# Kernel tuning notes

Hardware: AMD Instinct MI355X
Metric: run time of the kernel (lower is better)

Reference implementation:

```python
import jax, jax.numpy as jnp
import numpy as np
from jax import lax

SQRT_HALF = 0.7071067811865476
LAYERS = 20
STACKS = 2
LAYERS_PER_STACK = LAYERS // STACKS
K = 3
OUT_CH = 256
RES_CH = 64
GATE_CH = 128
SKIP_CH = 256
CIN_CH = 80


def setup_inputs() -> dict:
    key = jax.random.key(0)
    ks = jax.random.split(key, 20)
    s = 0.05
    inp = {
        'x': jax.random.normal(ks[0], (4, OUT_CH, 16384), jnp.float32),
        'c': jax.random.normal(ks[1], (4, CIN_CH, 16384), jnp.float32),
        # first conv: kernel size 2 (Conv1d2x1), out_channels -> residual_channels
        'W_first': jax.random.normal(ks[2], (RES_CH, OUT_CH, 2), jnp.float32) * s,
        'b_first': jnp.zeros((RES_CH,), jnp.float32),
        # per-layer dilated conv (residual -> gate), stacked over layers
        'W_dil': jax.random.normal(ks[3], (LAYERS, GATE_CH, RES_CH, K), jnp.float32) * s,
        'b_dil': jnp.zeros((LAYERS, GATE_CH), jnp.float32),
        # per-layer local-conditioning 1x1 (cin -> gate)
        'W_c': jax.random.normal(ks[4], (LAYERS, GATE_CH, CIN_CH), jnp.float32) * s,
        'b_c': jnp.zeros((LAYERS, GATE_CH), jnp.float32),
        # per-layer 1x1 skip (gate/2 -> skip) and out (gate/2 -> residual)
        'W_skip': jax.random.normal(ks[5], (LAYERS, SKIP_CH, GATE_CH // 2), jnp.float32) * s,
        'b_skip': jnp.zeros((LAYERS, SKIP_CH), jnp.float32),
        'W_out': jax.random.normal(ks[6], (LAYERS, RES_CH, GATE_CH // 2), jnp.float32) * s,
        'b_out': jnp.zeros((LAYERS, RES_CH), jnp.float32),
        # final 1x1 convs
        'W_last1': jax.random.normal(ks[7], (SKIP_CH, SKIP_CH), jnp.float32) * s,
        'b_last1': jnp.zeros((SKIP_CH,), jnp.float32),
        'W_last2': jax.random.normal(ks[8], (OUT_CH, SKIP_CH), jnp.float32) * s,
        'b_last2': jnp.zeros((OUT_CH,), jnp.float32),
    }
    return inp


def reference(x, c, W_first, b_first, W_dil, b_dil, W_c, b_c,
              W_skip, b_skip, W_out, b_out, W_last1, b_last1, W_last2, b_last2):
    dn = ('NCH', 'OIH', 'NCH')
    # first conv: F.pad(x, (1,0)) then kernel-2 conv == causal left pad 1
    h = lax.conv_general_dilated(x, W_first, (1,), [(1, 0)], dimension_numbers=dn)
    h = jnp.tanh(h + b_first[None, :, None])  # hparams.use_tanh_embed
    skips = None
    for l in range(LAYERS):
        d = 2 ** (l % LAYERS_PER_STACK)
        # causal dilated conv: pad left (K-1)*d
        y = lax.conv_general_dilated(h, W_dil[l], (1,), [((K - 1) * d, 0)],
                                     rhs_dilation=(d,), dimension_numbers=dn)
        y = y + b_dil[l][None, :, None]
        cond = jnp.einsum('bct,gc->bgt', c, W_c[l]) + b_c[l][None, :, None]
        a, b = jnp.split(y + cond, 2, axis=1)  # gated activation units
        z = jnp.tanh(a) * jax.nn.sigmoid(b)
        s = jnp.einsum('bgt,sg->bst', z, W_skip[l]) + b_skip[l][None, :, None]
        h = (jnp.einsum('bgt,rg->brt', z, W_out[l]) + b_out[l][None, :, None] + h) * SQRT_HALF
        if skips is None:
            skips = s
        else:
            skips = (skips + s) * SQRT_HALF  # faithful to original accumulation
    out = jax.nn.relu(skips)
    out = jnp.einsum('bst,os->bot', out, W_last1) + b_last1[None, :, None]
    out = jax.nn.relu(out)
    out = jnp.einsum('bst,os->bot', out, W_last2) + b_last2[None, :, None]
    return out
```

## Files before the change

### kernel.cpp

```cpp
#include <hip/hip_runtime.h>
#include <math.h>


#define T_LEN   16384
#define NB      4
#define BT      (NB * T_LEN)
#define NLAYERS 20
#define SQH     0.70710678118654752440f

typedef _Float16 half8 __attribute__((ext_vector_type(8)));
typedef _Float16 half4 __attribute__((ext_vector_type(4)));
typedef float f32x4 __attribute__((ext_vector_type(4)));

__device__ inline f32x4 mfma16(half8 a, half8 b, f32x4 c) {
  return __builtin_amdgcn_mfma_f32_16x16x32_f16(a, b, c, 0, 0, 0);
}

__global__ __launch_bounds__(256) void prep_pack(
    const float* __restrict__ Wf, const float* __restrict__ Wdil,
    const float* __restrict__ Wc, const float* __restrict__ Wskip,
    const float* __restrict__ Wout, const float* __restrict__ Wl1,
    const float* __restrict__ Wl2, const float* __restrict__ bdil,
    const float* __restrict__ bc, const float* __restrict__ bskip,
    _Float16* __restrict__ wdp, _Float16* __restrict__ wcp,
    _Float16* __restrict__ wop, _Float16* __restrict__ wskp,
    _Float16* __restrict__ wfp, _Float16* __restrict__ wl1p,
    _Float16* __restrict__ wl2p, float* __restrict__ bde,
    float* __restrict__ bsk)
{
  const float Q = 0.70710678118654752440f;
  const int WDP_E = 20 * 3 * 128 * 64;
  const int WCP_E = 20 * 128 * 96;
  const int WOP_E = 20 * 64 * 64;
  const int WSK_E = 256 * 1280;
  const int WFP_E = 64 * 512;
  const int WL_E  = 256 * 256;
  const int BDE_E = 20 * 128;
  const int BSK_E = 256;
  const int TOTAL = WDP_E + WCP_E + WOP_E + WSK_E + WFP_E + 2 * WL_E + BDE_E + BSK_E;
  for (int i = blockIdx.x * blockDim.x + threadIdx.x; i < TOTAL;
       i += gridDim.x * blockDim.x) {
    int j = i;
    if (j < WDP_E) {
      int l = j / (3 * 128 * 64); int r2 = j % (3 * 128 * 64);
      int tau = r2 / (128 * 64);  int r3 = r2 % (128 * 64);
      int n = r3 >> 6; int kc = r3 & 63;
      wdp[j] = (_Float16)Wdil[((l * 128 + n) * 64 + kc) * 3 + tau];
      continue;
    }
    j -= WDP_E;
    if (j < WCP_E) {
      int l = j / (128 * 96); int r2 = j % (128 * 96);
      int n = r2 / 96; int kc = r2 % 96;
      wcp[j] = (_Float16)(kc < 80 ? Wc[(l * 128 + n) * 80 + kc] : 0.f);
      continue;
    }
    j -= WCP_E;
    if (j < WOP_E) {
      int l = j >> 12; int r2 = j & 4095;
      int n = r2 >> 6; int kc = r2 & 63;
      wop[j] = (_Float16)Wout[(l * 64 + n) * 64 + kc];
      continue;
    }
    j -= WOP_E;
    if (j < WSK_E) {
      int n = j / 1280; int k = j % 1280;
      int l = k >> 6; int kc = k & 63;
      float f = (l == 0) ? 1.f : powf(Q, (float)(1 - l));
      wskp[j] = (_Float16)(Wskip[(l * 256 + n) * 64 + kc] * f);
      continue;
    }
    j -= WSK_E;
    if (j < WFP_E) {
      int n = j >> 9; int k = j & 511;
      int tau = k >> 8; int ci = k & 255;
      wfp[j] = (_Float16)Wf[(n * 256 + ci) * 2 + tau];
      continue;
    }
    j -= WFP_E;
    if (j < WL_E) { wl1p[j] = (_Float16)Wl1[j]; continue; }
    j -= WL_E;
    if (j < WL_E) { wl2p[j] = (_Float16)Wl2[j]; continue; }
    j -= WL_E;
    if (j < BDE_E) { bde[j] = bdil[j] + bc[j]; continue; }
    j -= BDE_E;
    {
      int n = j;
      float s = 0.f;
      for (int l = 0; l < NLAYERS; ++l) {
        float w = powf(Q, (float)(l == 0 ? 19 : 20 - l));
        s += bskip[l * 256 + n] * w;
      }
      bsk[n] = s;
    }
  }
}

__global__ __launch_bounds__(256) void tr_kernel(
    const float* __restrict__ src, _Float16* __restrict__ dst, int C, int Cpad, int CB)
{
  __shared__ float tile[32 * 33];
  int bid = blockIdx.x;
  int cb = bid % CB;
  int tb = (bid / CB) % (T_LEN / 32);
  int bb = bid / (CB * (T_LEN / 32));
  int t0 = tb * 32, ch0 = cb * 32;
  int tl = threadIdx.x & 31, cl = threadIdx.x >> 5;
#pragma unroll
  for (int i = 0; i < 4; ++i) {
    int ch = cl + 8 * i;
    float v = (ch0 + ch < C) ? src[((size_t)bb * C + ch0 + ch) * T_LEN + t0 + tl] : 0.f;
    tile[ch * 33 + tl] = v;
  }
  __syncthreads();
  int t = threadIdx.x >> 3;
  int c4 = (threadIdx.x & 7) * 4;
  half4 hv = {(_Float16)tile[(c4 + 0) * 33 + t], (_Float16)tile[(c4 + 1) * 33 + t],
              (_Float16)tile[(c4 + 2) * 33 + t], (_Float16)tile[(c4 + 3) * 33 + t]};
  *(half4*)&dst[((size_t)bb * T_LEN + t0 + t) * Cpad + ch0 + c4] = hv;
}

__global__ __launch_bounds__(256, 4) void first_conv(
    const _Float16* __restrict__ xt, const _Float16* __restrict__ wfp,
    const float* __restrict__ bf, _Float16* __restrict__ h0)
{
  __shared__ _Float16 As[128 * 72];
  __shared__ _Float16 Bs[64 * 72];
  const int tid = threadIdx.x;
  const int lane = tid & 63, w = tid >> 6;
  const int wx = w & 1, wy = w >> 1;
  const int l15 = lane & 15, quad = lane >> 4;
  const int p0 = blockIdx.x * 128;
  const int b = p0 >> 14, t0 = p0 & (T_LEN - 1);
  const int r = tid >> 1, halfo = (tid & 1) * 32;

  f32x4 acc[4][2];
#pragma unroll
  for (int mi = 0; mi < 4; ++mi)
#pragma unroll
    for (int ni = 0; ni < 2; ++ni) { f32x4 z = {0.f, 0.f, 0.f, 0.f}; acc[mi][ni] = z; }

  for (int s = 0; s < 8; ++s) {
    int tau = s >> 2, ci0 = (s & 3) * 64;
    int ts = t0 + r - 1 + tau;
    if (ts >= 0) {
      const uint4* src = (const uint4*)(xt + ((size_t)(b * T_LEN + ts) * 256 + ci0 + halfo));
#pragma unroll
      for (int j = 0; j < 4; ++j) *(uint4*)&As[r * 72 + halfo + 8 * j] = src[j];
    } else {
      uint4 z = {0, 0, 0, 0};
#pragma unroll
      for (int j = 0; j < 4; ++j) *(uint4*)&As[r * 72 + halfo + 8 * j] = z;
    }
    if (tid < 128) {
      const uint4* s4 = (const uint4*)(wfp + ((size_t)r * 512 + tau * 256 + ci0 + halfo));
#pragma unroll
      for (int j = 0; j < 4; ++j) *(uint4*)&Bs[r * 72 + halfo + 8 * j] = s4[j];
    }
    __syncthreads();
#pragma unroll
    for (int kc = 0; kc < 2; ++kc) {
      const int k0 = kc * 32 + quad * 8;
      half8 af[4], bfr[2];
#pragma unroll
      for (int mi = 0; mi < 4; ++mi)
        af[mi] = *(const half8*)&As[(64 * wy + 16 * mi + l15) * 72 + k0];
#pragma unroll
      for (int ni = 0; ni < 2; ++ni)
        bfr[ni] = *(const half8*)&Bs[(32 * wx + 16 * ni + l15) * 72 + k0];
#pragma unroll
      for (int mi = 0; mi < 4; ++mi)
#pragma unroll
        for (int ni = 0; ni < 2; ++ni)
          acc[mi][ni] = mfma16(af[mi], bfr[ni], acc[mi][ni]);
    }
    __syncthreads();
  }
#pragma unroll
  for (int mi = 0; mi < 4; ++mi)
#pragma unroll
    for (int ni = 0; ni < 2; ++ni) {
      int col = 32 * wx + 16 * ni + l15;
      int rowb = 64 * wy + 16 * mi + quad * 4;
      float bo = bf[col];
      size_t base = ((size_t)p0 + rowb) * 64 + col;
#pragma unroll
      for (int reg = 0; reg < 4; ++reg) {
        float v = acc[mi][ni][reg] + bo;
        float e = __expf(2.f * v);
        h0[base + (size_t)64 * reg] = (_Float16)(1.f - 2.f * __builtin_amdgcn_rcpf(e + 1.f));
      }
    }
}

__global__ __launch_bounds__(512, 4) void layer_kernel(
    const _Float16* __restrict__ hprev, _Float16* __restrict__ hnext,
    const _Float16* __restrict__ ctp,
    const _Float16* __restrict__ wdp_l, const _Float16* __restrict__ wcp_l,
    const _Float16* __restrict__ wop_l,
    const float* __restrict__ bde_l, const float* __restrict__ bout_l,
    _Float16* __restrict__ zslot, int d)
{
  __shared__ _Float16 As[128 * 72];
  __shared__ _Float16 Bs[128 * 72];
  __shared__ float bde_s[128];

  const int tid = threadIdx.x;
  const int lane = tid & 63, w = tid >> 6;
  const int wx = w & 1, wy = w >> 1;
  const int l15 = lane & 15, quad = lane >> 4;
  const int p0 = blockIdx.x * 128;
  const int b = p0 >> 14, t0 = p0 & (T_LEN - 1);
  const int r2 = tid >> 2, qo = (tid & 3) * 16;
  const int o8 = (tid & 3) * 8;

  if (tid < 128) bde_s[tid] = bde_l[tid];

  f32x4 acc[2][4];
#pragma unroll
  for (int mi = 0; mi < 2; ++mi)
#pragma unroll
    for (int ni = 0; ni < 4; ++ni) { f32x4 z = {0.f, 0.f, 0.f, 0.f}; acc[mi][ni] = z; }

  for (int s = 0; s < 5; ++s) {
    if (s < 3) {
      int ts = t0 + r2 - (2 - s) * d;
      if (ts >= 0) {
        const uint4* src = (const uint4*)(hprev + ((size_t)(b * T_LEN + ts) * 64 + qo));
        *(uint4*)&As[r2 * 72 + qo] = src[0];
        *(uint4*)&As[r2 * 72 + qo + 8] = src[1];
      } else {
        uint4 z4 = {0, 0, 0, 0};
        *(uint4*)&As[r2 * 72 + qo] = z4;
        *(uint4*)&As[r2 * 72 + qo + 8] = z4;
      }
      const uint4* sb = (const uint4*)(wdp_l + ((size_t)s * 8192 + r2 * 64 + qo));
      *(uint4*)&Bs[r2 * 72 + qo] = sb[0];
      *(uint4*)&Bs[r2 * 72 + qo + 8] = sb[1];
    } else if (s == 3) {
      const uint4* sa = (const uint4*)(ctp + ((size_t)(p0 + r2) * 96 + qo));
      *(uint4*)&As[r2 * 72 + qo] = sa[0];
      *(uint4*)&As[r2 * 72 + qo + 8] = sa[1];
      const uint4* sb = (const uint4*)(wcp_l + ((size_t)r2 * 96 + qo));
      *(uint4*)&Bs[r2 * 72 + qo] = sb[0];
      *(uint4*)&Bs[r2 * 72 + qo + 8] = sb[1];
    } else {
      *(uint4*)&As[r2 * 72 + o8] = *(const uint4*)(ctp + ((size_t)(p0 + r2) * 96 + 64 + o8));
      *(uint4*)&Bs[r2 * 72 + o8] = *(const uint4*)(wcp_l + ((size_t)r2 * 96 + 64 + o8));
    }
    __syncthreads();
    const int nkc = (s == 4) ? 1 : 2;
    for (int kc = 0; kc < nkc; ++kc) {
      const int k0 = kc * 32 + quad * 8;
      half8 af[2], bfr[4];
#pragma unroll
      for (int mi = 0; mi < 2; ++mi)
        af[mi] = *(const half8*)&As[(32 * wy + 16 * mi + l15) * 72 + k0];
#pragma unroll
      for (int ni = 0; ni < 4; ++ni) {
        int ncol = 32 * wx + 16 * (ni & 1) + 64 * (ni >> 1);
        bfr[ni] = *(const half8*)&Bs[(ncol + l15) * 72 + k0];
      }
#pragma unroll
      for (int mi = 0; mi < 2; ++mi)
#pragma unroll
        for (int ni = 0; ni < 4; ++ni)
          acc[mi][ni] = mfma16(af[mi], bfr[ni], acc[mi][ni]);
    }
    __syncthreads();
  }

#pragma unroll
  for (int mi = 0; mi < 2; ++mi)
#pragma unroll
    for (int ni2 = 0; ni2 < 2; ++ni2) {
      int colb = 32 * wx + 16 * ni2 + l15;
      float ba = bde_s[colb], bb = bde_s[colb + 64];
#pragma unroll
      for (int reg = 0; reg < 4; ++reg) {
        float av = acc[mi][ni2][reg] + ba;
        float gv = acc[mi][ni2 + 2][reg] + bb;
        float ea = __expf(2.f * av);
        float th = 1.f - 2.f * __builtin_amdgcn_rcpf(ea + 1.f);
        float sg = __builtin_amdgcn_rcpf(1.f + __expf(-gv));
        As[(32 * wy + 16 * mi + quad * 4 + reg) * 72 + colb] = (_Float16)(th * sg);
      }
    }

  if (tid < 256) {
    int row = tid >> 2;
    const uint4* sb = (const uint4*)(wop_l + ((size_t)row * 64 + qo));
    *(uint4*)&Bs[row * 72 + qo] = sb[0];
    *(uint4*)&Bs[row * 72 + qo + 8] = sb[1];
  }
  __syncthreads();

  {
    uint4 v0 = *(const uint4*)&As[r2 * 72 + qo];
    uint4 v1 = *(const uint4*)&As[r2 * 72 + qo + 8];
    uint4* dst = (uint4*)(zslot + ((size_t)(p0 + r2) * 64 + qo));
    dst[0] = v0; dst[1] = v1;
  }

  f32x4 a4[2][2];
#pragma unroll
  for (int mi = 0; mi < 2; ++mi)
#pragma unroll
    for (int ni = 0; ni < 2; ++ni) { f32x4 z = {0.f, 0.f, 0.f, 0.f}; a4[mi][ni] = z; }
#pragma unroll
  for (int kc = 0; kc < 2; ++kc) {
    const int k0 = kc * 32 + quad * 8;
    half8 af[2], bfr[2];
#pragma unroll
    for (int mi = 0; mi < 2; ++mi)
      af[mi] = *(const half8*)&As[(32 * wy + 16 * mi + l15) * 72 + k0];
#pragma unroll
    for (int ni = 0; ni < 2; ++ni)
      bfr[ni] = *(const half8*)&Bs[(32 * wx + 16 * ni + l15) * 72 + k0];
#pragma unroll
    for (int mi = 0; mi < 2; ++mi)
#pragma unroll
      for (int ni = 0; ni < 2; ++ni)
        a4[mi][ni] = mfma16(af[mi], bfr[ni], a4[mi][ni]);
  }
#pragma unroll
  for (int mi = 0; mi < 2; ++mi)
#pragma unroll
    for (int ni = 0; ni < 2; ++ni) {
      int col = 32 * wx + 16 * ni + l15;
      int rowb = 32 * wy + 16 * mi + quad * 4;
      float bo = bout_l[col];
      size_t base = ((size_t)p0 + rowb) * 64 + col;
#pragma unroll
      for (int reg = 0; reg < 4; ++reg) {
        float hv = (float)hprev[base + (size_t)64 * reg];
        hnext[base + (size_t)64 * reg] = (_Float16)((a4[mi][ni][reg] + bo + hv) * SQH);
      }
    }
}

__global__ __launch_bounds__(256, 4) void flush_kernel(
    const _Float16* __restrict__ zbuf, const _Float16* __restrict__ wskp,
    _Float16* __restrict__ Abuf, const float* __restrict__ bsk,
    _Float16* __restrict__ skr, int l0, int g, int mode)
{
  __shared__ _Float16 As[128 * 72];
  __shared__ _Float16 Bs[128 * 72];
  const int tid = threadIdx.x;
  const int lane = tid & 63, w = tid >> 6;
  const int wx = w & 1, wy = w >> 1;
  const int l15 = lane & 15, quad = lane >> 4;
  const int p0 = blockIdx.x * 128;
  const int n0 = blockIdx.y * 128;
  const int r = tid >> 1, halfo = (tid & 1) * 32;

  f32x4 acc[4][4];
#pragma unroll
  for (int mi = 0; mi < 4; ++mi)
#pragma unroll
    for (int ni = 0; ni < 4; ++ni) { f32x4 z = {0.f, 0.f, 0.f, 0.f}; acc[mi][ni] = z; }

  for (int j = 0; j < g; ++j) {
    int l = l0 + j;
    const _Float16* zsl = zbuf + (size_t)(l & 7) * BT * 64;
    const uint4* sa = (const uint4*)(zsl + ((size_t)(p0 + r) * 64 + halfo));
#pragma unroll
    for (int jj = 0; jj < 4; ++jj) *(uint4*)&As[r * 72 + halfo + 8 * jj] = sa[jj];
    const uint4* sb = (const uint4*)(wskp + ((size_t)(n0 + r) * 1280 + l * 64 + halfo));
#pragma unroll
    for (int jj = 0; jj < 4; ++jj) *(uint4*)&Bs[r * 72 + halfo + 8 * jj] = sb[jj];
    __syncthreads();
#pragma unroll
    for (int kc = 0; kc < 2; ++kc) {
      const int k0 = kc * 32 + quad * 8;
      half8 af[4], bfr[4];
#pragma unroll
      for (int mi = 0; mi < 4; ++mi)
        af[mi] = *(const half8*)&As[(64 * wy + 16 * mi + l15) * 72 + k0];
#pragma unroll
      for (int ni = 0; ni < 4; ++ni)
        bfr[ni] = *(const half8*)&Bs[(64 * wx + 16 * ni + l15) * 72 + k0];
#pragma unroll
      for (int mi = 0; mi < 4; ++mi)
#pragma unroll
        for (int ni = 0; ni < 4; ++ni)
          acc[mi][ni] = mfma16(af[mi], bfr[ni], acc[mi][ni]);
    }
    __syncthreads();
  }
  const float Q19 = 0.0013810679320049757f;
#pragma unroll
  for (int mi = 0; mi < 4; ++mi)
#pragma unroll
    for (int ni = 0; ni < 4; ++ni) {
      int col = n0 + 64 * wx + 16 * ni + l15;
      int rowb = 64 * wy + 16 * mi + quad * 4;
      size_t base = ((size_t)p0 + rowb) * 256 + col;
      if (mode == 2) {
        float bb = bsk[col];
#pragma unroll
        for (int reg = 0; reg < 4; ++reg) {
          float v = (acc[mi][ni][reg] + (float)Abuf[base + (size_t)256 * reg]) * Q19 + bb;
          skr[base + (size_t)256 * reg] = (_Float16)(v > 0.f ? v : 0.f);
        }
      } else if (mode == 1) {
#pragma unroll
        for (int reg = 0; reg < 4; ++reg) {
          size_t a = base + (size_t)256 * reg;
          Abuf[a] = (_Float16)((float)Abuf[a] + acc[mi][ni][reg]);
        }
      } else {
#pragma unroll
        for (int reg = 0; reg < 4; ++reg)
          Abuf[base + (size_t)256 * reg] = (_Float16)acc[mi][ni][reg];
      }
    }
}

__global__ __launch_bounds__(256, 4) void gemm256(
    const _Float16* __restrict__ Asrc, const _Float16* __restrict__ Bp,
    const float* __restrict__ bias, void* __restrict__ dst, int mode)
{
  __shared__ _Float16 smem[2 * 128 * 72];
  _Float16* As = smem;
  _Float16* Bs = smem + 128 * 72;
  const int tid = threadIdx.x;
  const int lane = tid & 63, w = tid >> 6;
  const int wx = w & 1, wy = w >> 1;
  const int l15 = lane & 15, quad = lane >> 4;
  const int p0 = blockIdx.x * 128;
  const int n0 = blockIdx.y * 128;
  const int r = tid >> 1, halfo = (tid & 1) * 32;

  f32x4 acc[4][4];
#pragma unroll
  for (int mi = 0; mi < 4; ++mi)
#pragma unroll
    for (int ni = 0; ni < 4; ++ni) { f32x4 z = {0.f, 0.f, 0.f, 0.f}; acc[mi][ni] = z; }

  for (int c4 = 0; c4 < 4; ++c4) {
    int k0g = c4 * 64;
    const uint4* sa = (const uint4*)(Asrc + ((size_t)(p0 + r) * 256 + k0g + halfo));
#pragma unroll
    for (int jj = 0; jj < 4; ++jj) *(uint4*)&As[r * 72 + halfo + 8 * jj] = sa[jj];
    const uint4* sb = (const uint4*)(Bp + ((size_t)(n0 + r) * 256 + k0g + halfo));
#pragma unroll
    for (int jj = 0; jj < 4; ++jj) *(uint4*)&Bs[r * 72 + halfo + 8 * jj] = sb[jj];
    __syncthreads();
#pragma unroll
    for (int kc = 0; kc < 2; ++kc) {
      const int k0 = kc * 32 + quad * 8;
      half8 af[4], bfr[4];
#pragma unroll
      for (int mi = 0; mi < 4; ++mi)
        af[mi] = *(const half8*)&As[(64 * wy + 16 * mi + l15) * 72 + k0];
#pragma unroll
      for (int ni = 0; ni < 4; ++ni)
        bfr[ni] = *(const half8*)&Bs[(64 * wx + 16 * ni + l15) * 72 + k0];
#pragma unroll
      for (int mi = 0; mi < 4; ++mi)
#pragma unroll
        for (int ni = 0; ni < 4; ++ni)
          acc[mi][ni] = mfma16(af[mi], bfr[ni], acc[mi][ni]);
    }
    __syncthreads();
  }
  if (mode == 0) {
#pragma unroll
    for (int mi = 0; mi < 4; ++mi)
#pragma unroll
      for (int ni = 0; ni < 4; ++ni) {
        int col = n0 + 64 * wx + 16 * ni + l15;
        int rowb = 64 * wy + 16 * mi + quad * 4;
        float bv = bias[col];
        _Float16* o = (_Float16*)dst;
#pragma unroll
        for (int reg = 0; reg < 4; ++reg) {
          float v = acc[mi][ni][reg] + bv;
          o[((size_t)(p0 + rowb + reg)) * 256 + col] = (_Float16)(v > 0.f ? v : 0.f);
        }
      }
  } else {
    float* Ts = (float*)smem;
    const int b = p0 >> 14, t0g = p0 & (T_LEN - 1);
    for (int pass = 0; pass < 2; ++pass) {
      if (wx == pass) {
#pragma unroll
        for (int mi = 0; mi < 4; ++mi)
#pragma unroll
          for (int ni = 0; ni < 4; ++ni) {
            int col_l = 16 * ni + l15;
            float bv = bias[n0 + 64 * pass + col_l];
            int tl = 64 * wy + 16 * mi + quad * 4;
#pragma unroll
            for (int reg = 0; reg < 4; ++reg)
              Ts[col_l * 132 + tl + reg] = acc[mi][ni][reg] + bv;
          }
      }
      __syncthreads();
      {
        int col_l = tid >> 2;
        int tq = (tid & 3) * 32;
        float* o = (float*)dst + ((size_t)b * 256 + n0 + 64 * pass + col_l) * T_LEN + t0g + tq;
#pragma unroll
        for (int j = 0; j < 8; ++j)
          *(float4*)(o + 4 * j) = *(const float4*)&Ts[col_l * 132 + tq + 4 * j];
      }
      __syncthreads();
    }
  }
}

extern "C" void kernel_launch(void* const* d_in, const int* in_sizes, int n_in,
                              void* d_out, int out_size, void* d_ws, size_t ws_size,
                              hipStream_t stream)
{
  const float* x     = (const float*)d_in[0];
  const float* c     = (const float*)d_in[1];
  const float* Wf    = (const float*)d_in[2];
  const float* bf    = (const float*)d_in[3];
  const float* Wdil  = (const float*)d_in[4];
  const float* bdil  = (const float*)d_in[5];
  const float* Wc    = (const float*)d_in[6];
  const float* bc    = (const float*)d_in[7];
  const float* Wskip = (const float*)d_in[8];
  const float* bskip = (const float*)d_in[9];
  const float* Wout  = (const float*)d_in[10];
  const float* bout  = (const float*)d_in[11];
  const float* Wl1   = (const float*)d_in[12];
  const float* bl1   = (const float*)d_in[13];
  const float* Wl2   = (const float*)d_in[14];
  const float* bl2   = (const float*)d_in[15];

  char* base = (char*)d_ws;
  _Float16* zbuf = (_Float16*)base;
  _Float16* xt   = zbuf;
  _Float16* skr  = zbuf + (size_t)4 * BT * 64;
  _Float16* y1   = zbuf;
  _Float16* ctp  = (_Float16*)(base + 67108864);
  _Float16* hA   = (_Float16*)(base + 79691776);
  _Float16* hB   = (_Float16*)(base + 88080384);
  _Float16* wdp  = (_Float16*)(base + 96468992);
  _Float16* wcp  = wdp  + (size_t)20 * 3 * 128 * 64;
  _Float16* wop  = wcp  + (size_t)20 * 128 * 96;
  _Float16* wskp = wop  + (size_t)20 * 64 * 64;
  _Float16* wfp  = wskp + (size_t)256 * 1280;
  _Float16* wl1p = wfp  + (size_t)64 * 512;
  _Float16* wl2p = wl1p + (size_t)256 * 256;
  float*    bde  = (float*)(wl2p + (size_t)256 * 256);
  float*    bsk  = bde + 20 * 128;
  _Float16* Abuf = (_Float16*)d_out;

  prep_pack<<<2048, 256, 0, stream>>>(Wf, Wdil, Wc, Wskip, Wout, Wl1, Wl2,
                                      bdil, bc, bskip,
                                      wdp, wcp, wop, wskp, wfp, wl1p, wl2p,
                                      bde, bsk);
  tr_kernel<<<NB * (T_LEN / 32) * 8, 256, 0, stream>>>(x, xt, 256, 256, 8);
  tr_kernel<<<NB * (T_LEN / 32) * 3, 256, 0, stream>>>(c, ctp, 80, 96, 3);
  first_conv<<<512, 256, 0, stream>>>(xt, wfp, bf, hA);

  const _Float16* hin = hA;
  _Float16* hout = hB;
  for (int l = 0; l < NLAYERS; ++l) {
    int d = 1 << (l % 10);
    layer_kernel<<<512, 512, 0, stream>>>(
        hin, hout, ctp,
        wdp + (size_t)l * 3 * 128 * 64, wcp + (size_t)l * 128 * 96,
        wop + (size_t)l * 64 * 64, bde + l * 128, bout + l * 64,
        zbuf + (size_t)(l & 7) * BT * 64, d);
    _Float16* tmp = (_Float16*)hin; hin = hout; hout = tmp;
    if (l == 7)  flush_kernel<<<dim3(512, 2), 256, 0, stream>>>(zbuf, wskp, Abuf, bsk, skr, 0, 8, 0);
    if (l == 15) flush_kernel<<<dim3(512, 2), 256, 0, stream>>>(zbuf, wskp, Abuf, bsk, skr, 8, 8, 1);
    if (l == 19) flush_kernel<<<dim3(512, 2), 256, 0, stream>>>(zbuf, wskp, Abuf, bsk, skr, 16, 4, 2);
  }
  gemm256<<<dim3(512, 2), 256, 0, stream>>>(skr, wl1p, bl1, (void*)y1, 0);
  gemm256<<<dim3(512, 2), 256, 0, stream>>>(y1, wl2p, bl2, d_out, 1);
}
```

Measured before the change: 640.0 us.

## Swizzle block order across XCDs, widen x transpose, merge flush halves, skip dead last-layer residual

Adds an XCD-aware block-index swizzle to every kernel so neighbouring tiles land on the same chiplet's L2. Replaces the x transpose with a 128-wide-time tile kernel that uses float4 loads and half8 stores. The flush kernel now runs both 128-column output halves in one 512-thread block, so each z tile is loaded once and shared. The final layer also skips its residual output GEMM, whose result is never used. This trades extra shared memory in flush and more index arithmetic for less redundant global traffic.

```diff
diff --git a/kernel.cpp b/kernel.cpp
--- a/kernel.cpp
+++ b/kernel.cpp
@@ -14,6 +14,10 @@
 
 __device__ inline f32x4 mfma16(half8 a, half8 b, f32x4 c) {
   return __builtin_amdgcn_mfma_f32_16x16x32_f16(a, b, c, 0, 0, 0);
+}
+
+__device__ __forceinline__ int xswz(int pb, int nwg) {
+  return (pb & 7) * (nwg >> 3) + (pb >> 3);
 }
 
 __global__ __launch_bounds__(256) void prep_pack(
@@ -96,14 +100,45 @@
   }
 }
 
+__global__ __launch_bounds__(256) void tr_x_kernel(
+    const float* __restrict__ src, _Float16* __restrict__ dst)
+{
+  __shared__ float tile[32 * 132];
+  const int lb = xswz(blockIdx.x, 4096);
+  const int row_tile = lb >> 3, cb = lb & 7;
+  const int bb = row_tile >> 7;
+  const int t0 = (row_tile & 127) * 128;
+  const int ch0 = cb * 32;
+  {
+    int ch = threadIdx.x >> 3, tq = (threadIdx.x & 7) * 16;
+    const float4* s4 = (const float4*)(src + ((size_t)(bb * 256 + ch0 + ch)) * T_LEN + t0 + tq);
+#pragma unroll
+    for (int j = 0; j < 4; ++j)
+      *(float4*)&tile[ch * 132 + tq + 4 * j] = s4[j];
+  }
+  __syncthreads();
+  {
+    int t = threadIdx.x >> 1, c16 = (threadIdx.x & 1) * 16;
+    half8 h0, h1;
+#pragma unroll
+    for (int j = 0; j < 8; ++j) {
+      h0[j] = (_Float16)tile[(c16 + j) * 132 + t];
+      h1[j] = (_Float16)tile[(c16 + 8 + j) * 132 + t];
+    }
+    _Float16* o = dst + ((size_t)(bb * T_LEN + t0 + t)) * 256 + ch0 + c16;
+    *(half8*)o = h0;
+    *(half8*)(o + 8) = h1;
+  }
+}
+
 __global__ __launch_bounds__(256) void tr_kernel(
     const float* __restrict__ src, _Float16* __restrict__ dst, int C, int Cpad, int CB)
 {
   __shared__ float tile[32 * 33];
-  int bid = blockIdx.x;
-  int cb = bid % CB;
-  int tb = (bid / CB) % (T_LEN / 32);
-  int bb = bid / (CB * (T_LEN / 32));
+  int lb = xswz(blockIdx.x, gridDim.x);
+  int cb = lb % CB;
+  int tb = (lb / CB) % (T_LEN / 32);
+  int bb = lb / (CB * (T_LEN / 32));
   int t0 = tb * 32, ch0 = cb * 32;
   int tl = threadIdx.x & 31, cl = threadIdx.x >> 5;
 #pragma unroll
@@ -130,7 +165,7 @@
   const int lane = tid & 63, w = tid >> 6;
   const int wx = w & 1, wy = w >> 1;
   const int l15 = lane & 15, quad = lane >> 4;
-  const int p0 = blockIdx.x * 128;
+  const int p0 = xswz(blockIdx.x, 512) * 128;
   const int b = p0 >> 14, t0 = p0 & (T_LEN - 1);
   const int r = tid >> 1, halfo = (tid & 1) * 32;
 
@@ -199,7 +234,7 @@
     const _Float16* __restrict__ wdp_l, const _Float16* __restrict__ wcp_l,
     const _Float16* __restrict__ wop_l,
     const float* __restrict__ bde_l, const float* __restrict__ bout_l,
-    _Float16* __restrict__ zslot, int d)
+    _Float16* __restrict__ zslot, int d, int last)
 {
   __shared__ _Float16 As[128 * 72];
   __shared__ _Float16 Bs[128 * 72];
@@ -209,7 +244,7 @@
   const int lane = tid & 63, w = tid >> 6;
   const int wx = w & 1, wy = w >> 1;
   const int l15 = lane & 15, quad = lane >> 4;
-  const int p0 = blockIdx.x * 128;
+  const int p0 = xswz(blockIdx.x, 512) * 128;
   const int b = p0 >> 14, t0 = p0 & (T_LEN - 1);
   const int r2 = tid >> 2, qo = (tid & 3) * 16;
   const int o8 = (tid & 3) * 8;
@@ -287,7 +322,7 @@
       }
     }
 
-  if (tid < 256) {
+  if (!last && tid < 256) {
     int row = tid >> 2;
     const uint4* sb = (const uint4*)(wop_l + ((size_t)row * 64 + qo));
     *(uint4*)&Bs[row * 72 + qo] = sb[0];
@@ -302,6 +337,8 @@
     dst[0] = v0; dst[1] = v1;
   }
 
+  if (last) return;
+
   f32x4 a4[2][2];
 #pragma unroll
   for (int mi = 0; mi < 2; ++mi)
@@ -339,20 +376,24 @@
     }
 }
 
-__global__ __launch_bounds__(256, 4) void flush_kernel(
+__global__ __launch_bounds__(512, 4) void flush_kernel(
     const _Float16* __restrict__ zbuf, const _Float16* __restrict__ wskp,
     _Float16* __restrict__ Abuf, const float* __restrict__ bsk,
     _Float16* __restrict__ skr, int l0, int g, int mode)
 {
   __shared__ _Float16 As[128 * 72];
-  __shared__ _Float16 Bs[128 * 72];
+  __shared__ _Float16 Bs0[128 * 72];
+  __shared__ _Float16 Bs1[128 * 72];
   const int tid = threadIdx.x;
-  const int lane = tid & 63, w = tid >> 6;
-  const int wx = w & 1, wy = w >> 1;
+  const int half = tid >> 8;
+  _Float16* Bsh = half ? Bs1 : Bs0;
+  const int tloc = tid & 255;
+  const int lane = tloc & 63, w4 = tloc >> 6;
+  const int wx = w4 & 1, wy = w4 >> 1;
   const int l15 = lane & 15, quad = lane >> 4;
-  const int p0 = blockIdx.x * 128;
-  const int n0 = blockIdx.y * 128;
-  const int r = tid >> 1, halfo = (tid & 1) * 32;
+  const int p0 = xswz(blockIdx.x, 512) * 128;
+  const int n0 = half * 128;
+  const int r = tloc >> 1, halfo = (tloc & 1) * 32;
 
   f32x4 acc[4][4];
 #pragma unroll
@@ -360,15 +401,18 @@
 #pragma unroll
     for (int ni = 0; ni < 4; ++ni) { f32x4 z = {0.f, 0.f, 0.f, 0.f}; acc[mi][ni] = z; }
 
+#pragma unroll 1
   for (int j = 0; j < g; ++j) {
-    int l = l0 + j;
-    const _Float16* zsl = zbuf + (size_t)(l & 7) * BT * 64;
-    const uint4* sa = (const uint4*)(zsl + ((size_t)(p0 + r) * 64 + halfo));
-#pragma unroll
-    for (int jj = 0; jj < 4; ++jj) *(uint4*)&As[r * 72 + halfo + 8 * jj] = sa[jj];
-    const uint4* sb = (const uint4*)(wskp + ((size_t)(n0 + r) * 1280 + l * 64 + halfo));
-#pragma unroll
-    for (int jj = 0; jj < 4; ++jj) *(uint4*)&Bs[r * 72 + halfo + 8 * jj] = sb[jj];
+    const int lj = l0 + j;
+    const _Float16* zsl = zbuf + (size_t)(lj & 7) * ((size_t)BT * 64);
+    if (half == 0) {
+      const uint4* sa = (const uint4*)(zsl + ((size_t)(p0 + r) * 64 + halfo));
+#pragma unroll
+      for (int jj = 0; jj < 4; ++jj) *(uint4*)&As[r * 72 + halfo + 8 * jj] = sa[jj];
+    }
+    const uint4* sb = (const uint4*)(wskp + ((size_t)(n0 + r) * 1280 + lj * 64 + halfo));
+#pragma unroll
+    for (int jj = 0; jj < 4; ++jj) *(uint4*)&Bsh[r * 72 + halfo + 8 * jj] = sb[jj];
     __syncthreads();
 #pragma unroll
     for (int kc = 0; kc < 2; ++kc) {
@@ -379,7 +423,7 @@
         af[mi] = *(const half8*)&As[(64 * wy + 16 * mi + l15) * 72 + k0];
 #pragma unroll
       for (int ni = 0; ni < 4; ++ni)
-        bfr[ni] = *(const half8*)&Bs[(64 * wx + 16 * ni + l15) * 72 + k0];
+        bfr[ni] = *(const half8*)&Bsh[(64 * wx + 16 * ni + l15) * 72 + k0];
 #pragma unroll
       for (int mi = 0; mi < 4; ++mi)
 #pragma unroll
@@ -428,7 +472,7 @@
   const int lane = tid & 63, w = tid >> 6;
   const int wx = w & 1, wy = w >> 1;
   const int l15 = lane & 15, quad = lane >> 4;
-  const int p0 = blockIdx.x * 128;
+  const int p0 = xswz(blockIdx.x, 512) * 128;
   const int n0 = blockIdx.y * 128;
   const int r = tid >> 1, halfo = (tid & 1) * 32;
 
@@ -555,7 +599,7 @@
                                       bdil, bc, bskip,
                                       wdp, wcp, wop, wskp, wfp, wl1p, wl2p,
                                       bde, bsk);
-  tr_kernel<<<NB * (T_LEN / 32) * 8, 256, 0, stream>>>(x, xt, 256, 256, 8);
+  tr_x_kernel<<<4096, 256, 0, stream>>>(x, xt);
   tr_kernel<<<NB * (T_LEN / 32) * 3, 256, 0, stream>>>(c, ctp, 80, 96, 3);
   first_conv<<<512, 256, 0, stream>>>(xt, wfp, bf, hA);
 
@@ -567,11 +611,11 @@
         hin, hout, ctp,
         wdp + (size_t)l * 3 * 128 * 64, wcp + (size_t)l * 128 * 96,
         wop + (size_t)l * 64 * 64, bde + l * 128, bout + l * 64,
-        zbuf + (size_t)(l & 7) * BT * 64, d);
+        zbuf + (size_t)(l & 7) * BT * 64, d, (l == NLAYERS - 1) ? 1 : 0);
     _Float16* tmp = (_Float16*)hin; hin = hout; hout = tmp;
-    if (l == 7)  flush_kernel<<<dim3(512, 2), 256, 0, stream>>>(zbuf, wskp, Abuf, bsk, skr, 0, 8, 0);
-    if (l == 15) flush_kernel<<<dim3(512, 2), 256, 0, stream>>>(zbuf, wskp, Abuf, bsk, skr, 8, 8, 1);
-    if (l == 19) flush_kernel<<<dim3(512, 2), 256, 0, stream>>>(zbuf, wskp, Abuf, bsk, skr, 16, 4, 2);
+    if (l == 7)  flush_kernel<<<512, 512, 0, stream>>>(zbuf, wskp, Abuf, bsk, skr, 0, 8, 0);
+    if (l == 15) flush_kernel<<<512, 512, 0, stream>>>(zbuf, wskp, Abuf, bsk, skr, 8, 8, 1);
+    if (l == 19) flush_kernel<<<512, 512, 0, stream>>>(zbuf, wskp, Abuf, bsk, skr, 16, 4, 2);
   }
   gemm256<<<dim3(512, 2), 256, 0, stream>>>(skr, wl1p, bl1, (void*)y1, 0);
   gemm256<<<dim3(512, 2), 256, 0, stream>>>(y1, wl2p, bl2, d_out, 1);
```

Result: faster. 617.1 us (-3.6%).
